# Kernel tuning notes

Measured on AMD Instinct MI355X. Metric: run time of the kernel, lower is better.

The kernel has to match this reference:

```python
import jax, jax.numpy as jnp
import numpy as np

L, V, D, H, F, S = 6, 32000, 768, 12, 3072, 1024
B, T = 2, 1024
DK = D // H
EPS = 1e-5  # torch LayerNorm default


def _ln(x, w, b):
    m = x.mean(-1, keepdims=True)
    v = ((x - m) ** 2).mean(-1, keepdims=True)
    return (x - m) / jnp.sqrt(v + EPS) * w + b


def setup_inputs() -> dict:
    key = jax.random.key(0)
    ks = jax.random.split(key, 16)
    n = lambda k, shape: jax.random.normal(k, shape, jnp.float32) * 0.02
    return {
        "x": jax.random.randint(ks[0], (B, T), 0, V),
        "tok_emb": n(ks[1], (V, D)),
        "pos_emb": n(ks[2], (S, D)),
        "ln1_w": jnp.ones((L, D), jnp.float32), "ln1_b": jnp.zeros((L, D), jnp.float32),
        "wq": n(ks[3], (L, D, D)), "bq": jnp.zeros((L, D), jnp.float32),
        "wk": n(ks[4], (L, D, D)), "bk": jnp.zeros((L, D), jnp.float32),
        "wv": n(ks[5], (L, D, D)), "bv": jnp.zeros((L, D), jnp.float32),
        "wo": n(ks[6], (L, D, D)), "bo": jnp.zeros((L, D), jnp.float32),
        "ln2_w": jnp.ones((L, D), jnp.float32), "ln2_b": jnp.zeros((L, D), jnp.float32),
        "w1": n(ks[7], (L, F, D)), "b1": jnp.zeros((L, F), jnp.float32),
        "w2": n(ks[8], (L, D, F)), "b2": jnp.zeros((L, D), jnp.float32),
        "lnf_w": jnp.ones((D,), jnp.float32), "lnf_b": jnp.zeros((D,), jnp.float32),
        "head_w": n(ks[9], (V, D)),
    }


def reference(x, tok_emb, pos_emb, ln1_w, ln1_b, wq, bq, wk, bk, wv, bv, wo, bo,
              ln2_w, ln2_b, w1, b1, w2, b2, lnf_w, lnf_b, head_w):
    Bx, Tx = x.shape
    h = tok_emb[x] + pos_emb[:Tx]                     # [B,T,D]
    causal = jnp.triu(jnp.ones((Tx, Tx), bool), 1)    # True above diagonal
    scale = 1.0 / np.sqrt(DK)
    for i in range(L):
        a = _ln(h, ln1_w[i], ln1_b[i])
        q = (a @ wq[i].T + bq[i]).reshape(Bx, Tx, H, DK).transpose(0, 2, 1, 3)
        k = (a @ wk[i].T + bk[i]).reshape(Bx, Tx, H, DK).transpose(0, 2, 1, 3)
        v = (a @ wv[i].T + bv[i]).reshape(Bx, Tx, H, DK).transpose(0, 2, 1, 3)
        scores = jnp.einsum("bhtd,bhsd->bhts", q, k) * scale  # [B,H,T,T]
        scores = jnp.where(causal, -jnp.inf, scores)
        attn = jax.nn.softmax(scores, axis=-1)
        ctx = jnp.einsum("bhts,bhsd->bhtd", attn, v)
        ctx = ctx.transpose(0, 2, 1, 3).reshape(Bx, Tx, D)
        h = h + ctx @ wo[i].T + bo[i]
        f = _ln(h, ln2_w[i], ln2_b[i])
        h = h + jax.nn.relu(f @ w1[i].T + b1[i]) @ w2[i].T + b2[i]
    h = _ln(h, lnf_w, lnf_b)
    return h @ head_w.T                               # [B,T,V] logits
```

## Files before the change

kernel.cpp:

```cpp
#include <hip/hip_runtime.h>

typedef unsigned short u16;
typedef __bf16 bf16x8 __attribute__((ext_vector_type(8)));
typedef float f32x4 __attribute__((ext_vector_type(4)));
typedef float f32x4v __attribute__((ext_vector_type(4)));
typedef u16 u16x4 __attribute__((ext_vector_type(4)));

__device__ __forceinline__ float bf2f(u16 u) {
    unsigned x = ((unsigned)u) << 16;
    return __builtin_bit_cast(float, x);
}
__device__ __forceinline__ u16 f2bf(float f) {
    unsigned x = __builtin_bit_cast(unsigned, f);
    unsigned r = (x + 0x7FFFu + ((x >> 16) & 1u)) >> 16;
    return (u16)r;
}

__global__ __launch_bounds__(256) void cvt_kernel(const float* __restrict__ in,
                                                  u16* __restrict__ out, long n,
                                                  long chunk, long stride) {
    for (long i = (long)blockIdx.x * 1024 + (long)threadIdx.x * 4; i < n;
         i += (long)gridDim.x * 1024) {
        f32x4v v = *(const f32x4v*)(in + i);
        u16x4 o;
        o.x = f2bf(v.x); o.y = f2bf(v.y); o.z = f2bf(v.z); o.w = f2bf(v.w);
        long c = i / chunk, rrem = i - c * chunk;
        *(u16x4*)(out + c * stride + rrem) = o;
    }
}

__global__ __launch_bounds__(256) void bias_fuse_kernel(const float* __restrict__ bq,
                                                        const float* __restrict__ bk,
                                                        const float* __restrict__ bv,
                                                        float* __restrict__ dst) {
    int i = blockIdx.x * 256 + threadIdx.x;
    if (i < 6 * 768) {
        int l = i / 768, j = i % 768;
        dst[l * 2304 + j] = bq[i];
        dst[l * 2304 + 768 + j] = bk[i];
        dst[l * 2304 + 1536 + j] = bv[i];
    }
}

__global__ __launch_bounds__(256) void embed_ln_kernel(
    const int* __restrict__ x, const float* __restrict__ tok,
    const float* __restrict__ pos, float* __restrict__ h,
    const float* __restrict__ w, const float* __restrict__ b,
    u16* __restrict__ out) {
    __shared__ float red[4];
    int row = blockIdx.x;
    int t = row & 1023;
    long id = x[row];
    const float* te = tok + id * 768L;
    const float* pe = pos + (long)t * 768L;
    float* hr = h + (long)row * 768L;
    int tid = threadIdx.x, lane = tid & 63, wid = tid >> 6;
    float v0 = te[tid] + pe[tid];
    float v1 = te[tid + 256] + pe[tid + 256];
    float v2 = te[tid + 512] + pe[tid + 512];
    hr[tid] = v0; hr[tid + 256] = v1; hr[tid + 512] = v2;
    float s = v0 + v1 + v2;
    for (int o = 32; o; o >>= 1) s += __shfl_xor(s, o);
    if (lane == 0) red[wid] = s;
    __syncthreads();
    float mean = (red[0] + red[1] + red[2] + red[3]) * (1.f / 768.f);
    __syncthreads();
    float d0 = v0 - mean, d1 = v1 - mean, d2 = v2 - mean;
    float q = d0 * d0 + d1 * d1 + d2 * d2;
    for (int o = 32; o; o >>= 1) q += __shfl_xor(q, o);
    if (lane == 0) red[wid] = q;
    __syncthreads();
    float var = (red[0] + red[1] + red[2] + red[3]) * (1.f / 768.f);
    float rstd = rsqrtf(var + 1e-5f);
    u16* orow = out + (long)row * 768L;
    orow[tid]       = f2bf(d0 * rstd * w[tid]       + b[tid]);
    orow[tid + 256] = f2bf(d1 * rstd * w[tid + 256] + b[tid + 256]);
    orow[tid + 512] = f2bf(d2 * rstd * w[tid + 512] + b[tid + 512]);
}

__global__ __launch_bounds__(192) void redln_kernel(
    const float* __restrict__ part, long pstride, int S,
    const float* __restrict__ bias, float* __restrict__ h,
    const float* __restrict__ w, const float* __restrict__ b,
    u16* __restrict__ out) {
    __shared__ float red[3];
    int row = blockIdx.x;
    int tid = threadIdx.x, lane = tid & 63, wid = tid >> 6;
    long base = (long)row * 768 + tid * 4;
    f32x4v x = *(const f32x4v*)(h + base);
    f32x4v bb = *(const f32x4v*)(bias + tid * 4);
    x += bb;
    for (int s = 0; s < S; s++) x += *(const f32x4v*)(part + (long)s * pstride + base);
    *(f32x4v*)(h + base) = x;
    float s = x.x + x.y + x.z + x.w;
    for (int o = 32; o; o >>= 1) s += __shfl_xor(s, o);
    if (lane == 0) red[wid] = s;
    __syncthreads();
    float mean = (red[0] + red[1] + red[2]) * (1.f / 768.f);
    __syncthreads();
    f32x4v d = x - mean;
    float q = d.x * d.x + d.y * d.y + d.z * d.z + d.w * d.w;
    for (int o = 32; o; o >>= 1) q += __shfl_xor(q, o);
    if (lane == 0) red[wid] = q;
    __syncthreads();
    float var = (red[0] + red[1] + red[2]) * (1.f / 768.f);
    float rstd = rsqrtf(var + 1e-5f);
    f32x4v wv = *(const f32x4v*)(w + tid * 4);
    f32x4v bv = *(const f32x4v*)(b + tid * 4);
    u16x4 o;
    o.x = f2bf(d.x * rstd * wv.x + bv.x);
    o.y = f2bf(d.y * rstd * wv.y + bv.y);
    o.z = f2bf(d.z * rstd * wv.z + bv.z);
    o.w = f2bf(d.w * rstd * wv.w + bv.w);
    *(u16x4*)(out + base) = o;
}

__global__ __launch_bounds__(256) void flash_kernel(
    const u16* __restrict__ qkv,
    const u16* __restrict__ vT,
    u16* __restrict__ ctx) {
    int z = blockIdx.z;
    int zb = z / 12, zh = z - zb * 12;
    int qt = (int)gridDim.x - 1 - (int)blockIdx.x;
    int q0 = qt * 64;
    int tid = threadIdx.x, lane = tid & 63, wid = tid >> 6;
    int rA = lane & 15, sA = lane >> 4;

    const u16* Qbase = qkv + (long)zb * 1024 * 2304 + zh * 64;
    const u16* Kbase = Qbase + 768;
    const u16* Vbase = vT + (long)z * 64 * 1024;

    __shared__ u16 Ks[64 * 64];
    __shared__ u16 Vs[64 * 64];
    __shared__ u16 Ps[4][16 * 64];

    bf16x8 aq[2];
    {
        const u16* qrow = Qbase + (long)(q0 + wid * 16 + rA) * 2304;
        aq[0] = *(const bf16x8*)(qrow + sA * 8);
        aq[1] = *(const bf16x8*)(qrow + 32 + sA * 8);
    }

    float m[4], l[4];
    f32x4 acc_o[4];
#pragma unroll
    for (int j = 0; j < 4; j++) { m[j] = -1e30f; l[j] = 0.f; }
#pragma unroll
    for (int nf = 0; nf < 4; nf++) acc_o[nf] = 0.f;

    int grow0 = q0 + wid * 16 + sA * 4;
    int nkv = qt + 1;
    for (int t = 0; t < nkv; ++t) {
        int kv0 = t * 64;
#pragma unroll
        for (int c0 = 0; c0 < 512; c0 += 256) {
            int c = c0 + tid;
            int row = c >> 3, half = (c >> 2) & 1, sl = c & 3;
            int ks = sl ^ ((row >> 1) & 3);
            __builtin_amdgcn_global_load_lds(
                (const __attribute__((address_space(1))) unsigned*)(Kbase + (long)(kv0 + row) * 2304 + half * 32 + ks * 8),
                (__attribute__((address_space(3))) unsigned*)(Ks + c * 8), 16, 0, 0);
        }
#pragma unroll
        for (int c0 = 0; c0 < 512; c0 += 256) {
            int c = c0 + tid;
            int row = c >> 3, half = (c >> 2) & 1, sl = c & 3;
            int ks = sl ^ ((row >> 1) & 3);
            __builtin_amdgcn_global_load_lds(
                (const __attribute__((address_space(1))) unsigned*)(Vbase + (long)row * 1024 + kv0 + half * 32 + ks * 8),
                (__attribute__((address_space(3))) unsigned*)(Vs + c * 8), 16, 0, 0);
        }
        __syncthreads();

        f32x4 s[4];
#pragma unroll
        for (int nf = 0; nf < 4; nf++) s[nf] = 0.f;
        __builtin_amdgcn_s_setprio(1);
#pragma unroll
        for (int h = 0; h < 2; h++)
#pragma unroll
            for (int nf = 0; nf < 4; nf++) {
                int row = nf * 16 + rA;
                bf16x8 bk_ = *(const bf16x8*)(Ks + row * 64 + h * 32 + ((sA ^ ((row >> 1) & 3))) * 8);
                s[nf] = __builtin_amdgcn_mfma_f32_16x16x32_bf16(aq[h], bk_, s[nf], 0, 0, 0);
            }
        __builtin_amdgcn_s_setprio(0);
#pragma unroll
        for (int nf = 0; nf < 4; nf++) {
            int col = kv0 + nf * 16 + rA;
#pragma unroll
            for (int j = 0; j < 4; j++)
                s[nf][j] = (col <= grow0 + j) ? s[nf][j] * 0.125f : -1e30f;
        }
        float pm[4];
#pragma unroll
        for (int j = 0; j < 4; j++) {
            float v = fmaxf(fmaxf(s[0][j], s[1][j]), fmaxf(s[2][j], s[3][j]));
#pragma unroll
            for (int o = 1; o < 16; o <<= 1) v = fmaxf(v, __shfl_xor(v, o));
            pm[j] = v;
        }
        float esc[4];
#pragma unroll
        for (int j = 0; j < 4; j++) {
            float mn = fmaxf(m[j], pm[j]);
            esc[j] = __expf(m[j] - mn);
            m[j] = mn;
        }
        float ts[4] = {0.f, 0.f, 0.f, 0.f};
#pragma unroll
        for (int nf = 0; nf < 4; nf++) {
            int c = nf * 16 + rA;
            int half = c >> 5, ch = (c >> 3) & 3, e = c & 7;
#pragma unroll
            for (int j = 0; j < 4; j++) {
                float p = __expf(s[nf][j] - m[j]);
                ts[j] += p;
                int r = sA * 4 + j;
                Ps[wid][r * 64 + half * 32 + (ch ^ ((r >> 1) & 3)) * 8 + e] = f2bf(p);
            }
        }
#pragma unroll
        for (int j = 0; j < 4; j++) {
            float v = ts[j];
#pragma unroll
            for (int o = 1; o < 16; o <<= 1) v += __shfl_xor(v, o);
            l[j] = l[j] * esc[j] + v;
        }
#pragma unroll
        for (int nf = 0; nf < 4; nf++)
#pragma unroll
            for (int j = 0; j < 4; j++) acc_o[nf][j] *= esc[j];

        __builtin_amdgcn_s_setprio(1);
#pragma unroll
        for (int h = 0; h < 2; h++) {
            bf16x8 ap = *(const bf16x8*)(Ps[wid] + rA * 64 + h * 32 + ((sA ^ ((rA >> 1) & 3))) * 8);
#pragma unroll
            for (int nf = 0; nf < 4; nf++) {
                int row = nf * 16 + rA;
                bf16x8 bv_ = *(const bf16x8*)(Vs + row * 64 + h * 32 + ((sA ^ ((row >> 1) & 3))) * 8);
                acc_o[nf] = __builtin_amdgcn_mfma_f32_16x16x32_bf16(ap, bv_, acc_o[nf], 0, 0, 0);
            }
        }
        __builtin_amdgcn_s_setprio(0);
        __syncthreads();
    }

    float inv[4];
#pragma unroll
    for (int j = 0; j < 4; j++) inv[j] = 1.f / l[j];
    u16* crow = ctx + ((long)zb * 1024 + q0 + wid * 16) * 768 + zh * 64;
#pragma unroll
    for (int nf = 0; nf < 4; nf++)
#pragma unroll
        for (int j = 0; j < 4; j++)
            crow[(long)(sA * 4 + j) * 768 + nf * 16 + rA] = f2bf(acc_o[nf][j] * inv[j]);
}

template <int BM, int BN, int BK, int EPI, int SK>
__global__ __launch_bounds__(256) void gemm8_kernel(
    const u16* __restrict__ A, int lda,
    const u16* __restrict__ Bm, int ldb,
    void* __restrict__ Cv, int ldc,
    const float* __restrict__ bias, int Kslice, int gm,
    u16* __restrict__ aux, long partStride) {
    constexpr int CPR = BK / 8;
    constexpr int KH = BK / 32;
    int flat = blockIdx.x;
    int tid = threadIdx.x;
    int nwg = gridDim.x;
    int qq = nwg >> 3, rr = nwg & 7;
    int xcd = flat & 7, wi = flat >> 3;
    int swz = (xcd < rr) ? (xcd * (qq + 1) + wi) : (rr * (qq + 1) + (xcd - rr) * qq + wi);
    int slice = 0, wblk = swz;
    if (SK > 1) { int nbs = nwg / SK; slice = swz / nbs; wblk = swz - slice * nbs; }
    int ntile = wblk / gm, mt = wblk - ntile * gm;
    int bm0 = mt * BM, bn0 = ntile * BN;
    long koff = (long)slice * Kslice;
    const u16* Ab = A + (long)bm0 * lda + koff;
    const u16* Bb = Bm + (long)bn0 * ldb + koff;

    __shared__ u16 As[2][BM * BK];
    __shared__ u16 Bs[2][BN * BK];

    int lane = tid & 63, wid = tid >> 6;
    constexpr int WM = BM / 2, WN = BN / 2, MR = WM / 16, NR = WN / 16;
    int wm0 = (wid >> 1) * WM, wn0 = (wid & 1) * WN;

    f32x4 acc[MR][NR];
#pragma unroll
    for (int mi = 0; mi < MR; mi++)
#pragma unroll
        for (int ni = 0; ni < NR; ni++) acc[mi][ni] = 0.f;

    int nt = Kslice / BK;

    auto key = [](int row) { return (BK == 32) ? ((row >> 1) & 3) : (row & 7); };

    auto stage = [&](int buf, int k0) {
        constexpr int CA = BM * CPR;
#pragma unroll
        for (int c0 = 0; c0 < CA; c0 += 256) {
            int c = c0 + tid;
            int row = c / CPR, sl = c & (CPR - 1);
            int ks = sl ^ key(row);
            __builtin_amdgcn_global_load_lds(
                (const __attribute__((address_space(1))) unsigned*)(Ab + (long)row * lda + k0 + ks * 8),
                (__attribute__((address_space(3))) unsigned*)(As[buf] + c * 8), 16, 0, 0);
        }
        constexpr int CB = BN * CPR;
#pragma unroll
        for (int c0 = 0; c0 < CB; c0 += 256) {
            int c = c0 + tid;
            int row = c / CPR, sl = c & (CPR - 1);
            int ks = sl ^ key(row);
            __builtin_amdgcn_global_load_lds(
                (const __attribute__((address_space(1))) unsigned*)(Bb + (long)row * ldb + k0 + ks * 8),
                (__attribute__((address_space(3))) unsigned*)(Bs[buf] + c * 8), 16, 0, 0);
        }
    };

    stage(0, 0);
    __syncthreads();
    int cur = 0;
    int rA = lane & 15, sA = lane >> 4;
    for (int t = 0; t < nt; ++t) {
        if (t + 1 < nt) stage(cur ^ 1, (t + 1) * BK);
        bf16x8 af[MR][KH], bfr[NR][KH];
#pragma unroll
        for (int mi = 0; mi < MR; mi++) {
            int row = wm0 + mi * 16 + rA;
#pragma unroll
            for (int h = 0; h < KH; h++)
                af[mi][h] = *(const bf16x8*)(As[cur] + row * BK + (((h << 2) + sA) ^ key(row)) * 8);
        }
#pragma unroll
        for (int ni = 0; ni < NR; ni++) {
            int row = wn0 + ni * 16 + rA;
#pragma unroll
            for (int h = 0; h < KH; h++)
                bfr[ni][h] = *(const bf16x8*)(Bs[cur] + row * BK + (((h << 2) + sA) ^ key(row)) * 8);
        }
#pragma unroll
        for (int h = 0; h < KH; h++)
#pragma unroll
            for (int mi = 0; mi < MR; mi++)
#pragma unroll
                for (int ni = 0; ni < NR; ni++)
                    acc[mi][ni] = __builtin_amdgcn_mfma_f32_16x16x32_bf16(
                        af[mi][h], bfr[ni][h], acc[mi][ni], 0, 0, 0);
        __syncthreads();
        cur ^= 1;
    }

#pragma unroll
    for (int mi = 0; mi < MR; mi++)
#pragma unroll
        for (int ni = 0; ni < NR; ni++) {
            int gmb = bm0 + wm0 + mi * 16 + ((lane >> 4) << 2);
            int gn = bn0 + wn0 + ni * 16 + (lane & 15);
            if (EPI == 6) {
                if (gn < 1536) {
#pragma unroll
                    for (int j = 0; j < 4; j++)
                        ((u16*)Cv)[(long)(gmb + j) * ldc + gn] =
                            f2bf(acc[mi][ni][j] + bias[gn]);
                } else {
                    u16x4 o;
#pragma unroll
                    for (int j = 0; j < 4; j++) o[j] = f2bf(acc[mi][ni][j] + bias[gn]);
                    int hh = (gn - 1536) >> 6, dk = gn & 63;
                    long off = ((long)((gmb >> 10) * 12 + hh) * 64 + dk) * 1024 + (gmb & 1023);
                    *(u16x4*)(aux + off) = o;
                }
            } else {
#pragma unroll
                for (int j = 0; j < 4; j++) {
                    float v = acc[mi][ni][j];
                    long idx = (long)(gmb + j) * ldc + gn;
                    if (EPI == 2) ((u16*)Cv)[idx] = f2bf(fmaxf(v + bias[gn], 0.f));
                    else ((float*)Cv)[(long)slice * partStride + idx] = v;
                }
            }
        }
}

extern "C" void kernel_launch(void* const* d_in, const int* in_sizes, int n_in,
                              void* d_out, int out_size, void* d_ws, size_t ws_size,
                              hipStream_t stream) {
    const int L = 6, D = 768, F = 3072, T = 1024, V = 32000;
    const int M = 2048;
    const int* x = (const int*)d_in[0];
    const float* tok = (const float*)d_in[1];
    const float* pos = (const float*)d_in[2];
    const float* ln1w = (const float*)d_in[3];
    const float* ln1b = (const float*)d_in[4];
    const float* wq = (const float*)d_in[5];
    const float* bq = (const float*)d_in[6];
    const float* wk = (const float*)d_in[7];
    const float* bk = (const float*)d_in[8];
    const float* wv = (const float*)d_in[9];
    const float* bv = (const float*)d_in[10];
    const float* wo = (const float*)d_in[11];
    const float* bo = (const float*)d_in[12];
    const float* ln2w = (const float*)d_in[13];
    const float* ln2b = (const float*)d_in[14];
    const float* w1 = (const float*)d_in[15];
    const float* b1 = (const float*)d_in[16];
    const float* w2 = (const float*)d_in[17];
    const float* b2 = (const float*)d_in[18];
    const float* lnfw = (const float*)d_in[19];
    const float* lnfb = (const float*)d_in[20];
    const float* headw = (const float*)d_in[21];

    char* p = (char*)d_ws;
    auto alloc = [&](size_t bytes) {
        char* r = p;
        p += (bytes + 255) & ~(size_t)255;
        return r;
    };
    const long DD = (long)D * D, FD = (long)F * D;
    const long PS = (long)M * D;
    u16* qkvw_b = (u16*)alloc(L * 3 * DD * 2);
    u16* wo_b = (u16*)alloc(L * DD * 2);
    u16* w1_b = (u16*)alloc(L * FD * 2);
    u16* w2_b = (u16*)alloc(L * FD * 2);
    u16* hw_b = (u16*)alloc((long)V * D * 2);
    float* qkvbias = (float*)alloc(L * 2304 * 4);
    float* h = (float*)alloc((long)M * D * 4);
    u16* a = (u16*)alloc((long)M * D * 2);
    u16* qkvb = (u16*)alloc((long)M * 2304 * 2);
    u16* vT = (u16*)alloc(24L * 64 * T * 2);
    u16* ctxb = (u16*)alloc((long)M * D * 2);
    u16* f1 = (u16*)alloc((long)M * F * 2);
    float* part = (float*)alloc(4L * PS * 4);

    auto cvt = [&](const float* src, u16* dst, long n, long chunk, long stride) {
        long blocks = (n + 1023) / 1024;
        if (blocks > 4096) blocks = 4096;
        cvt_kernel<<<dim3((unsigned)blocks), 256, 0, stream>>>(src, dst, n, chunk, stride);
    };
    cvt(wq, qkvw_b, L * DD, DD, 3 * DD);
    cvt(wk, qkvw_b + DD, L * DD, DD, 3 * DD);
    cvt(wv, qkvw_b + 2 * DD, L * DD, DD, 3 * DD);
    cvt(wo, wo_b, L * DD, L * DD, L * DD);
    cvt(w1, w1_b, L * FD, L * FD, L * FD);
    cvt(w2, w2_b, L * FD, L * FD, L * FD);
    cvt(headw, hw_b, (long)V * D, (long)V * D, (long)V * D);
    bias_fuse_kernel<<<dim3(18), 256, 0, stream>>>(bq, bk, bv, qkvbias);
    embed_ln_kernel<<<dim3(M), 256, 0, stream>>>(x, tok, pos, h, ln1w, ln1b, a);

    for (int i = 0; i < L; i++) {
        int nx = i + 1;
        bool hn = nx < L;
        gemm8_kernel<64, 128, 64, 6, 1><<<dim3(576), 256, 0, stream>>>(
            a, D, qkvw_b + i * 3 * DD, D, qkvb, 2304, qkvbias + i * 2304,
            D, 32, vT, 0);
        flash_kernel<<<dim3(16, 1, 24), 256, 0, stream>>>(qkvb, vT, ctxb);
        gemm8_kernel<64, 128, 64, 5, 2><<<dim3(384), 256, 0, stream>>>(
            ctxb, D, wo_b + i * DD, D, part, D, nullptr, 384, 32, nullptr, PS);
        redln_kernel<<<dim3(M), 192, 0, stream>>>(
            part, PS, 2, bo + i * D, h, ln2w + i * D, ln2b + i * D, a);
        gemm8_kernel<64, 128, 64, 2, 1><<<dim3(768), 256, 0, stream>>>(
            a, D, w1_b + i * FD, D, f1, F, b1 + i * F, D, 32, nullptr, 0);
        gemm8_kernel<64, 128, 64, 5, 4><<<dim3(768), 256, 0, stream>>>(
            f1, F, w2_b + i * FD, F, part, D, nullptr, 768, 32, nullptr, PS);
        redln_kernel<<<dim3(M), 192, 0, stream>>>(
            part, PS, 4, b2 + i * D, h,
            hn ? ln1w + nx * D : lnfw, hn ? ln1b + nx * D : lnfb, a);
    }
    gemm8_kernel<128, 128, 32, 5, 1><<<dim3(4000), 256, 0, stream>>>(
        a, D, hw_b, D, d_out, V, nullptr, D, 16, nullptr, 0);
}
```

Before: 979.3 us.

## Fuse split-K reduce and LayerNorm into GEMM tail; double-buffer flash K/V

Removes the separate redln kernel and instead has the last-arriving split-K GEMM block for each 64-row tile (tracked by an atomic counter) add the partials, bias and residual, then compute LayerNorm and write bf16 output. It also double-buffers the K/V LDS tiles in the flash attention kernel so the next tile's loads are issued before the current tile is computed. This saves kernel launches and a full pass over h and the partials, and lets global loads overlap with MFMA work. The costs are a serialized tail in one block per row tile, variance computed as E[x²]−mean², and a possible race in the flash kernel because there is no barrier between loading the next tile and reading the current one.

```diff
diff --git a/kernel.cpp b/kernel.cpp
--- a/kernel.cpp
+++ b/kernel.cpp
@@ -78,43 +78,6 @@
     orow[tid + 512] = f2bf(d2 * rstd * w[tid + 512] + b[tid + 512]);
 }
 
-__global__ __launch_bounds__(192) void redln_kernel(
-    const float* __restrict__ part, long pstride, int S,
-    const float* __restrict__ bias, float* __restrict__ h,
-    const float* __restrict__ w, const float* __restrict__ b,
-    u16* __restrict__ out) {
-    __shared__ float red[3];
-    int row = blockIdx.x;
-    int tid = threadIdx.x, lane = tid & 63, wid = tid >> 6;
-    long base = (long)row * 768 + tid * 4;
-    f32x4v x = *(const f32x4v*)(h + base);
-    f32x4v bb = *(const f32x4v*)(bias + tid * 4);
-    x += bb;
-    for (int s = 0; s < S; s++) x += *(const f32x4v*)(part + (long)s * pstride + base);
-    *(f32x4v*)(h + base) = x;
-    float s = x.x + x.y + x.z + x.w;
-    for (int o = 32; o; o >>= 1) s += __shfl_xor(s, o);
-    if (lane == 0) red[wid] = s;
-    __syncthreads();
-    float mean = (red[0] + red[1] + red[2]) * (1.f / 768.f);
-    __syncthreads();
-    f32x4v d = x - mean;
-    float q = d.x * d.x + d.y * d.y + d.z * d.z + d.w * d.w;
-    for (int o = 32; o; o >>= 1) q += __shfl_xor(q, o);
-    if (lane == 0) red[wid] = q;
-    __syncthreads();
-    float var = (red[0] + red[1] + red[2]) * (1.f / 768.f);
-    float rstd = rsqrtf(var + 1e-5f);
-    f32x4v wv = *(const f32x4v*)(w + tid * 4);
-    f32x4v bv = *(const f32x4v*)(b + tid * 4);
-    u16x4 o;
-    o.x = f2bf(d.x * rstd * wv.x + bv.x);
-    o.y = f2bf(d.y * rstd * wv.y + bv.y);
-    o.z = f2bf(d.z * rstd * wv.z + bv.z);
-    o.w = f2bf(d.w * rstd * wv.w + bv.w);
-    *(u16x4*)(out + base) = o;
-}
-
 __global__ __launch_bounds__(256) void flash_kernel(
     const u16* __restrict__ qkv,
     const u16* __restrict__ vT,
@@ -130,8 +93,8 @@
     const u16* Kbase = Qbase + 768;
     const u16* Vbase = vT + (long)z * 64 * 1024;
 
-    __shared__ u16 Ks[64 * 64];
-    __shared__ u16 Vs[64 * 64];
+    __shared__ u16 Ks[2][64 * 64];
+    __shared__ u16 Vs[2][64 * 64];
     __shared__ u16 Ps[4][16 * 64];
 
     bf16x8 aq[2];
@@ -141,17 +104,7 @@
         aq[1] = *(const bf16x8*)(qrow + 32 + sA * 8);
     }
 
-    float m[4], l[4];
-    f32x4 acc_o[4];
-#pragma unroll
-    for (int j = 0; j < 4; j++) { m[j] = -1e30f; l[j] = 0.f; }
-#pragma unroll
-    for (int nf = 0; nf < 4; nf++) acc_o[nf] = 0.f;
-
-    int grow0 = q0 + wid * 16 + sA * 4;
-    int nkv = qt + 1;
-    for (int t = 0; t < nkv; ++t) {
-        int kv0 = t * 64;
+    auto stage = [&](int buf, int kv0) {
 #pragma unroll
         for (int c0 = 0; c0 < 512; c0 += 256) {
             int c = c0 + tid;
@@ -159,7 +112,7 @@
             int ks = sl ^ ((row >> 1) & 3);
             __builtin_amdgcn_global_load_lds(
                 (const __attribute__((address_space(1))) unsigned*)(Kbase + (long)(kv0 + row) * 2304 + half * 32 + ks * 8),
-                (__attribute__((address_space(3))) unsigned*)(Ks + c * 8), 16, 0, 0);
+                (__attribute__((address_space(3))) unsigned*)(Ks[buf] + c * 8), 16, 0, 0);
         }
 #pragma unroll
         for (int c0 = 0; c0 < 512; c0 += 256) {
@@ -168,9 +121,26 @@
             int ks = sl ^ ((row >> 1) & 3);
             __builtin_amdgcn_global_load_lds(
                 (const __attribute__((address_space(1))) unsigned*)(Vbase + (long)row * 1024 + kv0 + half * 32 + ks * 8),
-                (__attribute__((address_space(3))) unsigned*)(Vs + c * 8), 16, 0, 0);
-        }
-        __syncthreads();
+                (__attribute__((address_space(3))) unsigned*)(Vs[buf] + c * 8), 16, 0, 0);
+        }
+    };
+
+    float m[4], l[4];
+    f32x4 acc_o[4];
+#pragma unroll
+    for (int j = 0; j < 4; j++) { m[j] = -1e30f; l[j] = 0.f; }
+#pragma unroll
+    for (int nf = 0; nf < 4; nf++) acc_o[nf] = 0.f;
+
+    int grow0 = q0 + wid * 16 + sA * 4;
+    int nkv = qt + 1;
+
+    stage(0, 0);
+    __syncthreads();
+    for (int t = 0; t < nkv; ++t) {
+        int cur = t & 1;
+        int kv0 = t * 64;
+        if (t + 1 < nkv) stage(cur ^ 1, (t + 1) * 64);
 
         f32x4 s[4];
 #pragma unroll
@@ -181,7 +151,7 @@
 #pragma unroll
             for (int nf = 0; nf < 4; nf++) {
                 int row = nf * 16 + rA;
-                bf16x8 bk_ = *(const bf16x8*)(Ks + row * 64 + h * 32 + ((sA ^ ((row >> 1) & 3))) * 8);
+                bf16x8 bk_ = *(const bf16x8*)(Ks[cur] + row * 64 + h * 32 + ((sA ^ ((row >> 1) & 3))) * 8);
                 s[nf] = __builtin_amdgcn_mfma_f32_16x16x32_bf16(aq[h], bk_, s[nf], 0, 0, 0);
             }
         __builtin_amdgcn_s_setprio(0);
@@ -239,7 +209,7 @@
 #pragma unroll
             for (int nf = 0; nf < 4; nf++) {
                 int row = nf * 16 + rA;
-                bf16x8 bv_ = *(const bf16x8*)(Vs + row * 64 + h * 32 + ((sA ^ ((row >> 1) & 3))) * 8);
+                bf16x8 bv_ = *(const bf16x8*)(Vs[cur] + row * 64 + h * 32 + ((sA ^ ((row >> 1) & 3))) * 8);
                 acc_o[nf] = __builtin_amdgcn_mfma_f32_16x16x32_bf16(ap, bv_, acc_o[nf], 0, 0, 0);
             }
         }
@@ -259,12 +229,16 @@
 }
 
 template <int BM, int BN, int BK, int EPI, int SK>
-__global__ __launch_bounds__(256) void gemm8_kernel(
+__global__ __launch_bounds__(256) void gemm9_kernel(
     const u16* __restrict__ A, int lda,
     const u16* __restrict__ Bm, int ldb,
     void* __restrict__ Cv, int ldc,
     const float* __restrict__ bias, int Kslice, int gm,
-    u16* __restrict__ aux, long partStride) {
+    u16* __restrict__ aux, long partStride,
+    int* __restrict__ cnt, int tailNeed, int tailS,
+    const float* __restrict__ tbias, float* __restrict__ th,
+    const float* __restrict__ tw, const float* __restrict__ tb,
+    u16* __restrict__ tout) {
     constexpr int CPR = BK / 8;
     constexpr int KH = BK / 32;
     int flat = blockIdx.x;
@@ -283,6 +257,7 @@
 
     __shared__ u16 As[2][BM * BK];
     __shared__ u16 Bs[2][BN * BK];
+    __shared__ int isLast;
 
     int lane = tid & 63, wid = tid >> 6;
     constexpr int WM = BM / 2, WN = BN / 2, MR = WM / 16, NR = WN / 16;
@@ -384,6 +359,53 @@
                 }
             }
         }
+
+    if (EPI == 5 && tailNeed > 0) {
+        __syncthreads();
+        if (tid == 0) {
+            __threadfence();
+            int old = atomicAdd(cnt + mt, 1);
+            isLast = (old == tailNeed - 1) ? 1 : 0;
+        }
+        __syncthreads();
+        if (isLast) {
+            __threadfence();
+            const float* part = (const float*)Cv;
+            int r = tid >> 2, sub = tid & 3;
+            long rowbase = (long)(mt * 64 + r) * 768;
+            int col0 = sub * 192;
+            float sum = 0.f, sq = 0.f;
+#pragma unroll 4
+            for (int j = 0; j < 48; j++) {
+                long e = rowbase + col0 + j * 4;
+                f32x4v xv = *(const f32x4v*)(th + e);
+                xv += *(const f32x4v*)(tbias + col0 + j * 4);
+                for (int s = 0; s < tailS; s++)
+                    xv += *(const f32x4v*)(part + (long)s * partStride + e);
+                *(f32x4v*)(th + e) = xv;
+                sum += xv.x + xv.y + xv.z + xv.w;
+                sq += xv.x * xv.x + xv.y * xv.y + xv.z * xv.z + xv.w * xv.w;
+            }
+            sum += __shfl_xor(sum, 1); sum += __shfl_xor(sum, 2);
+            sq += __shfl_xor(sq, 1);  sq += __shfl_xor(sq, 2);
+            float mean = sum * (1.f / 768.f);
+            float var = sq * (1.f / 768.f) - mean * mean;
+            float rstd = rsqrtf(var + 1e-5f);
+#pragma unroll 4
+            for (int j = 0; j < 48; j++) {
+                long e = rowbase + col0 + j * 4;
+                f32x4v xv = *(const f32x4v*)(th + e);
+                f32x4v wv = *(const f32x4v*)(tw + col0 + j * 4);
+                f32x4v bv = *(const f32x4v*)(tb + col0 + j * 4);
+                u16x4 o;
+                o.x = f2bf((xv.x - mean) * rstd * wv.x + bv.x);
+                o.y = f2bf((xv.y - mean) * rstd * wv.y + bv.y);
+                o.z = f2bf((xv.z - mean) * rstd * wv.z + bv.z);
+                o.w = f2bf((xv.w - mean) * rstd * wv.w + bv.w);
+                *(u16x4*)(tout + e) = o;
+            }
+        }
+    }
 }
 
 extern "C" void kernel_launch(void* const* d_in, const int* in_sizes, int n_in,
@@ -435,6 +457,9 @@
     u16* ctxb = (u16*)alloc((long)M * D * 2);
     u16* f1 = (u16*)alloc((long)M * F * 2);
     float* part = (float*)alloc(4L * PS * 4);
+    int* cnts = (int*)alloc(12 * 32 * 4);
+
+    hipMemsetAsync(cnts, 0, 12 * 32 * 4, stream);
 
     auto cvt = [&](const float* src, u16* dst, long n, long chunk, long stride) {
         long blocks = (n + 1023) / 1024;
@@ -454,22 +479,23 @@
     for (int i = 0; i < L; i++) {
         int nx = i + 1;
         bool hn = nx < L;
-        gemm8_kernel<64, 128, 64, 6, 1><<<dim3(576), 256, 0, stream>>>(
+        gemm9_kernel<64, 128, 64, 6, 1><<<dim3(576), 256, 0, stream>>>(
             a, D, qkvw_b + i * 3 * DD, D, qkvb, 2304, qkvbias + i * 2304,
-            D, 32, vT, 0);
+            D, 32, vT, 0, nullptr, 0, 0, nullptr, nullptr, nullptr, nullptr, nullptr);
         flash_kernel<<<dim3(16, 1, 24), 256, 0, stream>>>(qkvb, vT, ctxb);
-        gemm8_kernel<64, 128, 64, 5, 2><<<dim3(384), 256, 0, stream>>>(
-            ctxb, D, wo_b + i * DD, D, part, D, nullptr, 384, 32, nullptr, PS);
-        redln_kernel<<<dim3(M), 192, 0, stream>>>(
-            part, PS, 2, bo + i * D, h, ln2w + i * D, ln2b + i * D, a);
-        gemm8_kernel<64, 128, 64, 2, 1><<<dim3(768), 256, 0, stream>>>(
-            a, D, w1_b + i * FD, D, f1, F, b1 + i * F, D, 32, nullptr, 0);
-        gemm8_kernel<64, 128, 64, 5, 4><<<dim3(768), 256, 0, stream>>>(
-            f1, F, w2_b + i * FD, F, part, D, nullptr, 768, 32, nullptr, PS);
-        redln_kernel<<<dim3(M), 192, 0, stream>>>(
-            part, PS, 4, b2 + i * D, h,
+        gemm9_kernel<64, 128, 64, 5, 2><<<dim3(384), 256, 0, stream>>>(
+            ctxb, D, wo_b + i * DD, D, part, D, nullptr, 384, 32, nullptr, PS,
+            cnts + (i * 2) * 32, 12, 2, bo + i * D, h,
+            ln2w + i * D, ln2b + i * D, a);
+        gemm9_kernel<64, 128, 64, 2, 1><<<dim3(768), 256, 0, stream>>>(
+            a, D, w1_b + i * FD, D, f1, F, b1 + i * F, D, 32, nullptr, 0,
+            nullptr, 0, 0, nullptr, nullptr, nullptr, nullptr, nullptr);
+        gemm9_kernel<64, 128, 64, 5, 4><<<dim3(768), 256, 0, stream>>>(
+            f1, F, w2_b + i * FD, F, part, D, nullptr, 768, 32, nullptr, PS,
+            cnts + (i * 2 + 1) * 32, 24, 4, b2 + i * D, h,
             hn ? ln1w + nx * D : lnfw, hn ? ln1b + nx * D : lnfb, a);
     }
-    gemm8_kernel<128, 128, 32, 5, 1><<<dim3(4000), 256, 0, stream>>>(
-        a, D, hw_b, D, d_out, V, nullptr, D, 16, nullptr, 0);
-}
+    gemm9_kernel<128, 128, 32, 5, 1><<<dim3(4000), 256, 0, stream>>>(
+        a, D, hw_b, D, d_out, V, nullptr, D, 16, nullptr, 0,
+        nullptr, 0, 0, nullptr, nullptr, nullptr, nullptr, nullptr);
+}
```

Measured after the change: 2.137 ms. 118% more time.

## Fuse all transformer layers into one persistent cooperative kernel with grid syncs

Applied to the files above, without the earlier changes.

Replaces the per-layer sequence of QKV GEMM, flash attention, output GEMM, residual-LayerNorm, FFN GEMMs and LayerNorm launches with a single cooperative persistent kernel. Blocks loop over job indices for each stage and call grid.sync between stages. The aim is to remove launch gaps and tail effects across the 42 small launches. The flash attention loop also gains double-buffered K/V staging so the next tile loads while the current one is computed. In exchange it adds grid-wide barrier cost, caps occupancy at a fixed blocks-per-CU value, and forces every stage to share one register and LDS budget.

```diff
diff --git a/kernel.cpp b/kernel.cpp
--- a/kernel.cpp
+++ b/kernel.cpp
@@ -1,4 +1,6 @@
 #include <hip/hip_runtime.h>
+#include <hip/hip_cooperative_groups.h>
+namespace cg = cooperative_groups;
 
 typedef unsigned short u16;
 typedef __bf16 bf16x8 __attribute__((ext_vector_type(8)));
@@ -78,188 +80,11 @@
     orow[tid + 512] = f2bf(d2 * rstd * w[tid + 512] + b[tid + 512]);
 }
 
-__global__ __launch_bounds__(192) void redln_kernel(
-    const float* __restrict__ part, long pstride, int S,
-    const float* __restrict__ bias, float* __restrict__ h,
-    const float* __restrict__ w, const float* __restrict__ b,
-    u16* __restrict__ out) {
-    __shared__ float red[3];
-    int row = blockIdx.x;
-    int tid = threadIdx.x, lane = tid & 63, wid = tid >> 6;
-    long base = (long)row * 768 + tid * 4;
-    f32x4v x = *(const f32x4v*)(h + base);
-    f32x4v bb = *(const f32x4v*)(bias + tid * 4);
-    x += bb;
-    for (int s = 0; s < S; s++) x += *(const f32x4v*)(part + (long)s * pstride + base);
-    *(f32x4v*)(h + base) = x;
-    float s = x.x + x.y + x.z + x.w;
-    for (int o = 32; o; o >>= 1) s += __shfl_xor(s, o);
-    if (lane == 0) red[wid] = s;
-    __syncthreads();
-    float mean = (red[0] + red[1] + red[2]) * (1.f / 768.f);
-    __syncthreads();
-    f32x4v d = x - mean;
-    float q = d.x * d.x + d.y * d.y + d.z * d.z + d.w * d.w;
-    for (int o = 32; o; o >>= 1) q += __shfl_xor(q, o);
-    if (lane == 0) red[wid] = q;
-    __syncthreads();
-    float var = (red[0] + red[1] + red[2]) * (1.f / 768.f);
-    float rstd = rsqrtf(var + 1e-5f);
-    f32x4v wv = *(const f32x4v*)(w + tid * 4);
-    f32x4v bv = *(const f32x4v*)(b + tid * 4);
-    u16x4 o;
-    o.x = f2bf(d.x * rstd * wv.x + bv.x);
-    o.y = f2bf(d.y * rstd * wv.y + bv.y);
-    o.z = f2bf(d.z * rstd * wv.z + bv.z);
-    o.w = f2bf(d.w * rstd * wv.w + bv.w);
-    *(u16x4*)(out + base) = o;
-}
-
-__global__ __launch_bounds__(256) void flash_kernel(
-    const u16* __restrict__ qkv,
-    const u16* __restrict__ vT,
-    u16* __restrict__ ctx) {
-    int z = blockIdx.z;
-    int zb = z / 12, zh = z - zb * 12;
-    int qt = (int)gridDim.x - 1 - (int)blockIdx.x;
-    int q0 = qt * 64;
-    int tid = threadIdx.x, lane = tid & 63, wid = tid >> 6;
-    int rA = lane & 15, sA = lane >> 4;
-
-    const u16* Qbase = qkv + (long)zb * 1024 * 2304 + zh * 64;
-    const u16* Kbase = Qbase + 768;
-    const u16* Vbase = vT + (long)z * 64 * 1024;
-
-    __shared__ u16 Ks[64 * 64];
-    __shared__ u16 Vs[64 * 64];
-    __shared__ u16 Ps[4][16 * 64];
-
-    bf16x8 aq[2];
-    {
-        const u16* qrow = Qbase + (long)(q0 + wid * 16 + rA) * 2304;
-        aq[0] = *(const bf16x8*)(qrow + sA * 8);
-        aq[1] = *(const bf16x8*)(qrow + 32 + sA * 8);
-    }
-
-    float m[4], l[4];
-    f32x4 acc_o[4];
-#pragma unroll
-    for (int j = 0; j < 4; j++) { m[j] = -1e30f; l[j] = 0.f; }
-#pragma unroll
-    for (int nf = 0; nf < 4; nf++) acc_o[nf] = 0.f;
-
-    int grow0 = q0 + wid * 16 + sA * 4;
-    int nkv = qt + 1;
-    for (int t = 0; t < nkv; ++t) {
-        int kv0 = t * 64;
-#pragma unroll
-        for (int c0 = 0; c0 < 512; c0 += 256) {
-            int c = c0 + tid;
-            int row = c >> 3, half = (c >> 2) & 1, sl = c & 3;
-            int ks = sl ^ ((row >> 1) & 3);
-            __builtin_amdgcn_global_load_lds(
-                (const __attribute__((address_space(1))) unsigned*)(Kbase + (long)(kv0 + row) * 2304 + half * 32 + ks * 8),
-                (__attribute__((address_space(3))) unsigned*)(Ks + c * 8), 16, 0, 0);
-        }
-#pragma unroll
-        for (int c0 = 0; c0 < 512; c0 += 256) {
-            int c = c0 + tid;
-            int row = c >> 3, half = (c >> 2) & 1, sl = c & 3;
-            int ks = sl ^ ((row >> 1) & 3);
-            __builtin_amdgcn_global_load_lds(
-                (const __attribute__((address_space(1))) unsigned*)(Vbase + (long)row * 1024 + kv0 + half * 32 + ks * 8),
-                (__attribute__((address_space(3))) unsigned*)(Vs + c * 8), 16, 0, 0);
-        }
-        __syncthreads();
-
-        f32x4 s[4];
-#pragma unroll
-        for (int nf = 0; nf < 4; nf++) s[nf] = 0.f;
-        __builtin_amdgcn_s_setprio(1);
-#pragma unroll
-        for (int h = 0; h < 2; h++)
-#pragma unroll
-            for (int nf = 0; nf < 4; nf++) {
-                int row = nf * 16 + rA;
-                bf16x8 bk_ = *(const bf16x8*)(Ks + row * 64 + h * 32 + ((sA ^ ((row >> 1) & 3))) * 8);
-                s[nf] = __builtin_amdgcn_mfma_f32_16x16x32_bf16(aq[h], bk_, s[nf], 0, 0, 0);
-            }
-        __builtin_amdgcn_s_setprio(0);
-#pragma unroll
-        for (int nf = 0; nf < 4; nf++) {
-            int col = kv0 + nf * 16 + rA;
-#pragma unroll
-            for (int j = 0; j < 4; j++)
-                s[nf][j] = (col <= grow0 + j) ? s[nf][j] * 0.125f : -1e30f;
-        }
-        float pm[4];
-#pragma unroll
-        for (int j = 0; j < 4; j++) {
-            float v = fmaxf(fmaxf(s[0][j], s[1][j]), fmaxf(s[2][j], s[3][j]));
-#pragma unroll
-            for (int o = 1; o < 16; o <<= 1) v = fmaxf(v, __shfl_xor(v, o));
-            pm[j] = v;
-        }
-        float esc[4];
-#pragma unroll
-        for (int j = 0; j < 4; j++) {
-            float mn = fmaxf(m[j], pm[j]);
-            esc[j] = __expf(m[j] - mn);
-            m[j] = mn;
-        }
-        float ts[4] = {0.f, 0.f, 0.f, 0.f};
-#pragma unroll
-        for (int nf = 0; nf < 4; nf++) {
-            int c = nf * 16 + rA;
-            int half = c >> 5, ch = (c >> 3) & 3, e = c & 7;
-#pragma unroll
-            for (int j = 0; j < 4; j++) {
-                float p = __expf(s[nf][j] - m[j]);
-                ts[j] += p;
-                int r = sA * 4 + j;
-                Ps[wid][r * 64 + half * 32 + (ch ^ ((r >> 1) & 3)) * 8 + e] = f2bf(p);
-            }
-        }
-#pragma unroll
-        for (int j = 0; j < 4; j++) {
-            float v = ts[j];
-#pragma unroll
-            for (int o = 1; o < 16; o <<= 1) v += __shfl_xor(v, o);
-            l[j] = l[j] * esc[j] + v;
-        }
-#pragma unroll
-        for (int nf = 0; nf < 4; nf++)
-#pragma unroll
-            for (int j = 0; j < 4; j++) acc_o[nf][j] *= esc[j];
-
-        __builtin_amdgcn_s_setprio(1);
-#pragma unroll
-        for (int h = 0; h < 2; h++) {
-            bf16x8 ap = *(const bf16x8*)(Ps[wid] + rA * 64 + h * 32 + ((sA ^ ((rA >> 1) & 3))) * 8);
-#pragma unroll
-            for (int nf = 0; nf < 4; nf++) {
-                int row = nf * 16 + rA;
-                bf16x8 bv_ = *(const bf16x8*)(Vs + row * 64 + h * 32 + ((sA ^ ((row >> 1) & 3))) * 8);
-                acc_o[nf] = __builtin_amdgcn_mfma_f32_16x16x32_bf16(ap, bv_, acc_o[nf], 0, 0, 0);
-            }
-        }
-        __builtin_amdgcn_s_setprio(0);
-        __syncthreads();
-    }
-
-    float inv[4];
-#pragma unroll
-    for (int j = 0; j < 4; j++) inv[j] = 1.f / l[j];
-    u16* crow = ctx + ((long)zb * 1024 + q0 + wid * 16) * 768 + zh * 64;
-#pragma unroll
-    for (int nf = 0; nf < 4; nf++)
-#pragma unroll
-        for (int j = 0; j < 4; j++)
-            crow[(long)(sA * 4 + j) * 768 + nf * 16 + rA] = f2bf(acc_o[nf][j] * inv[j]);
-}
 
 template <int BM, int BN, int BK, int EPI, int SK>
-__global__ __launch_bounds__(256) void gemm8_kernel(
+__device__ __forceinline__ void gemm_job(
+    int flat, int nwg, int tid,
+    u16* As0, u16* As1, u16* Bs0, u16* Bs1,
     const u16* __restrict__ A, int lda,
     const u16* __restrict__ Bm, int ldb,
     void* __restrict__ Cv, int ldc,
@@ -267,23 +92,17 @@
     u16* __restrict__ aux, long partStride) {
     constexpr int CPR = BK / 8;
     constexpr int KH = BK / 32;
-    int flat = blockIdx.x;
-    int tid = threadIdx.x;
-    int nwg = gridDim.x;
     int qq = nwg >> 3, rr = nwg & 7;
     int xcd = flat & 7, wi = flat >> 3;
     int swz = (xcd < rr) ? (xcd * (qq + 1) + wi) : (rr * (qq + 1) + (xcd - rr) * qq + wi);
     int slice = 0, wblk = swz;
-    if (SK > 1) { int nbs = nwg / SK; slice = swz / nbs; wblk = swz - slice * nbs; }
+    if (SK > 1) { int nbs = nwg / SK; slice = wblk / nbs; wblk -= slice * nbs; }
     int ntile = wblk / gm, mt = wblk - ntile * gm;
     int bm0 = mt * BM, bn0 = ntile * BN;
     long koff = (long)slice * Kslice;
     const u16* Ab = A + (long)bm0 * lda + koff;
     const u16* Bb = Bm + (long)bn0 * ldb + koff;
 
-    __shared__ u16 As[2][BM * BK];
-    __shared__ u16 Bs[2][BN * BK];
-
     int lane = tid & 63, wid = tid >> 6;
     constexpr int WM = BM / 2, WN = BN / 2, MR = WM / 16, NR = WN / 16;
     int wm0 = (wid >> 1) * WM, wn0 = (wid & 1) * WN;
@@ -295,10 +114,8 @@
         for (int ni = 0; ni < NR; ni++) acc[mi][ni] = 0.f;
 
     int nt = Kslice / BK;
-
     auto key = [](int row) { return (BK == 32) ? ((row >> 1) & 3) : (row & 7); };
-
-    auto stage = [&](int buf, int k0) {
+    auto stage = [&](u16* Asb, u16* Bsb, int k0) {
         constexpr int CA = BM * CPR;
 #pragma unroll
         for (int c0 = 0; c0 < CA; c0 += 256) {
@@ -307,7 +124,7 @@
             int ks = sl ^ key(row);
             __builtin_amdgcn_global_load_lds(
                 (const __attribute__((address_space(1))) unsigned*)(Ab + (long)row * lda + k0 + ks * 8),
-                (__attribute__((address_space(3))) unsigned*)(As[buf] + c * 8), 16, 0, 0);
+                (__attribute__((address_space(3))) unsigned*)(Asb + c * 8), 16, 0, 0);
         }
         constexpr int CB = BN * CPR;
 #pragma unroll
@@ -317,30 +134,31 @@
             int ks = sl ^ key(row);
             __builtin_amdgcn_global_load_lds(
                 (const __attribute__((address_space(1))) unsigned*)(Bb + (long)row * ldb + k0 + ks * 8),
-                (__attribute__((address_space(3))) unsigned*)(Bs[buf] + c * 8), 16, 0, 0);
+                (__attribute__((address_space(3))) unsigned*)(Bsb + c * 8), 16, 0, 0);
         }
     };
 
-    stage(0, 0);
-    __syncthreads();
-    int cur = 0;
+    stage(As0, Bs0, 0);
+    __syncthreads();
     int rA = lane & 15, sA = lane >> 4;
     for (int t = 0; t < nt; ++t) {
-        if (t + 1 < nt) stage(cur ^ 1, (t + 1) * BK);
+        u16* Asc = (t & 1) ? As1 : As0;
+        u16* Bsc = (t & 1) ? Bs1 : Bs0;
+        if (t + 1 < nt) stage((t & 1) ? As0 : As1, (t & 1) ? Bs0 : Bs1, (t + 1) * BK);
         bf16x8 af[MR][KH], bfr[NR][KH];
 #pragma unroll
         for (int mi = 0; mi < MR; mi++) {
             int row = wm0 + mi * 16 + rA;
 #pragma unroll
             for (int h = 0; h < KH; h++)
-                af[mi][h] = *(const bf16x8*)(As[cur] + row * BK + (((h << 2) + sA) ^ key(row)) * 8);
+                af[mi][h] = *(const bf16x8*)(Asc + row * BK + (((h << 2) + sA) ^ key(row)) * 8);
         }
 #pragma unroll
         for (int ni = 0; ni < NR; ni++) {
             int row = wn0 + ni * 16 + rA;
 #pragma unroll
             for (int h = 0; h < KH; h++)
-                bfr[ni][h] = *(const bf16x8*)(Bs[cur] + row * BK + (((h << 2) + sA) ^ key(row)) * 8);
+                bfr[ni][h] = *(const bf16x8*)(Bsc + row * BK + (((h << 2) + sA) ^ key(row)) * 8);
         }
 #pragma unroll
         for (int h = 0; h < KH; h++)
@@ -351,7 +169,6 @@
                     acc[mi][ni] = __builtin_amdgcn_mfma_f32_16x16x32_bf16(
                         af[mi][h], bfr[ni][h], acc[mi][ni], 0, 0, 0);
         __syncthreads();
-        cur ^= 1;
     }
 
 #pragma unroll
@@ -384,6 +201,267 @@
                 }
             }
         }
+}
+
+__device__ __forceinline__ void flash_job(
+    int job, int tid, u16* lds,
+    const u16* __restrict__ qkv, const u16* __restrict__ vT,
+    u16* __restrict__ ctx) {
+    int z = job >> 4;
+    int zb = z / 12, zh = z - zb * 12;
+    int qt = 15 - (job & 15);
+    int q0 = qt * 64;
+    int lane = tid & 63, wid = tid >> 6;
+    int rA = lane & 15, sA = lane >> 4;
+
+    u16* Ks0 = lds;            u16* Ks1 = lds + 4096;
+    u16* Vs0 = lds + 8192;     u16* Vs1 = lds + 12288;
+    u16* Psw = lds + 16384 + wid * 1024;
+
+    const u16* Qbase = qkv + (long)zb * 1024 * 2304 + zh * 64;
+    const u16* Kbase = Qbase + 768;
+    const u16* Vbase = vT + (long)z * 64 * 1024;
+
+    bf16x8 aq[2];
+    {
+        const u16* qrow = Qbase + (long)(q0 + wid * 16 + rA) * 2304;
+        aq[0] = *(const bf16x8*)(qrow + sA * 8);
+        aq[1] = *(const bf16x8*)(qrow + 32 + sA * 8);
+    }
+
+    auto stage = [&](u16* Ksb, u16* Vsb, int kv0) {
+#pragma unroll
+        for (int c0 = 0; c0 < 512; c0 += 256) {
+            int c = c0 + tid;
+            int row = c >> 3, half = (c >> 2) & 1, sl = c & 3;
+            int ks = sl ^ ((row >> 1) & 3);
+            __builtin_amdgcn_global_load_lds(
+                (const __attribute__((address_space(1))) unsigned*)(Kbase + (long)(kv0 + row) * 2304 + half * 32 + ks * 8),
+                (__attribute__((address_space(3))) unsigned*)(Ksb + c * 8), 16, 0, 0);
+        }
+#pragma unroll
+        for (int c0 = 0; c0 < 512; c0 += 256) {
+            int c = c0 + tid;
+            int row = c >> 3, half = (c >> 2) & 1, sl = c & 3;
+            int ks = sl ^ ((row >> 1) & 3);
+            __builtin_amdgcn_global_load_lds(
+                (const __attribute__((address_space(1))) unsigned*)(Vbase + (long)row * 1024 + kv0 + half * 32 + ks * 8),
+                (__attribute__((address_space(3))) unsigned*)(Vsb + c * 8), 16, 0, 0);
+        }
+    };
+
+    float m[4], l[4];
+    f32x4 acc_o[4];
+#pragma unroll
+    for (int j = 0; j < 4; j++) { m[j] = -1e30f; l[j] = 0.f; }
+#pragma unroll
+    for (int nf = 0; nf < 4; nf++) acc_o[nf] = 0.f;
+
+    int grow0 = q0 + wid * 16 + sA * 4;
+    int nkv = qt + 1;
+
+    stage(Ks0, Vs0, 0);
+    __syncthreads();
+    for (int t = 0; t < nkv; ++t) {
+        u16* Ksc = (t & 1) ? Ks1 : Ks0;
+        u16* Vsc = (t & 1) ? Vs1 : Vs0;
+        int kv0 = t * 64;
+        if (t + 1 < nkv) stage((t & 1) ? Ks0 : Ks1, (t & 1) ? Vs0 : Vs1, (t + 1) * 64);
+
+        f32x4 s[4];
+#pragma unroll
+        for (int nf = 0; nf < 4; nf++) s[nf] = 0.f;
+        __builtin_amdgcn_s_setprio(1);
+#pragma unroll
+        for (int h = 0; h < 2; h++)
+#pragma unroll
+            for (int nf = 0; nf < 4; nf++) {
+                int row = nf * 16 + rA;
+                bf16x8 bk_ = *(const bf16x8*)(Ksc + row * 64 + h * 32 + ((sA ^ ((row >> 1) & 3))) * 8);
+                s[nf] = __builtin_amdgcn_mfma_f32_16x16x32_bf16(aq[h], bk_, s[nf], 0, 0, 0);
+            }
+        __builtin_amdgcn_s_setprio(0);
+#pragma unroll
+        for (int nf = 0; nf < 4; nf++) {
+            int col = kv0 + nf * 16 + rA;
+#pragma unroll
+            for (int j = 0; j < 4; j++)
+                s[nf][j] = (col <= grow0 + j) ? s[nf][j] * 0.125f : -1e30f;
+        }
+        float pm[4];
+#pragma unroll
+        for (int j = 0; j < 4; j++) {
+            float v = fmaxf(fmaxf(s[0][j], s[1][j]), fmaxf(s[2][j], s[3][j]));
+#pragma unroll
+            for (int o = 1; o < 16; o <<= 1) v = fmaxf(v, __shfl_xor(v, o));
+            pm[j] = v;
+        }
+        float esc[4];
+#pragma unroll
+        for (int j = 0; j < 4; j++) {
+            float mn = fmaxf(m[j], pm[j]);
+            esc[j] = __expf(m[j] - mn);
+            m[j] = mn;
+        }
+        float ts[4] = {0.f, 0.f, 0.f, 0.f};
+#pragma unroll
+        for (int nf = 0; nf < 4; nf++) {
+            int c = nf * 16 + rA;
+            int half = c >> 5, ch = (c >> 3) & 3, e = c & 7;
+#pragma unroll
+            for (int j = 0; j < 4; j++) {
+                float p = __expf(s[nf][j] - m[j]);
+                ts[j] += p;
+                int r = sA * 4 + j;
+                Psw[r * 64 + half * 32 + (ch ^ ((r >> 1) & 3)) * 8 + e] = f2bf(p);
+            }
+        }
+#pragma unroll
+        for (int j = 0; j < 4; j++) {
+            float v = ts[j];
+#pragma unroll
+            for (int o = 1; o < 16; o <<= 1) v += __shfl_xor(v, o);
+            l[j] = l[j] * esc[j] + v;
+        }
+#pragma unroll
+        for (int nf = 0; nf < 4; nf++)
+#pragma unroll
+            for (int j = 0; j < 4; j++) acc_o[nf][j] *= esc[j];
+
+        __builtin_amdgcn_s_setprio(1);
+#pragma unroll
+        for (int h = 0; h < 2; h++) {
+            bf16x8 ap = *(const bf16x8*)(Psw + rA * 64 + h * 32 + ((sA ^ ((rA >> 1) & 3))) * 8);
+#pragma unroll
+            for (int nf = 0; nf < 4; nf++) {
+                int row = nf * 16 + rA;
+                bf16x8 bv_ = *(const bf16x8*)(Vsc + row * 64 + h * 32 + ((sA ^ ((row >> 1) & 3))) * 8);
+                acc_o[nf] = __builtin_amdgcn_mfma_f32_16x16x32_bf16(ap, bv_, acc_o[nf], 0, 0, 0);
+            }
+        }
+        __builtin_amdgcn_s_setprio(0);
+        __syncthreads();
+    }
+
+    float inv[4];
+#pragma unroll
+    for (int j = 0; j < 4; j++) inv[j] = 1.f / l[j];
+    u16* crow = ctx + ((long)zb * 1024 + q0 + wid * 16) * 768 + zh * 64;
+#pragma unroll
+    for (int nf = 0; nf < 4; nf++)
+#pragma unroll
+        for (int j = 0; j < 4; j++)
+            crow[(long)(sA * 4 + j) * 768 + nf * 16 + rA] = f2bf(acc_o[nf][j] * inv[j]);
+}
+
+__device__ __forceinline__ void redln_row(
+    int row, int tid, float* red,
+    const float* __restrict__ part, long pstride, int S,
+    const float* __restrict__ bias, float* __restrict__ h,
+    const float* __restrict__ w, const float* __restrict__ b,
+    u16* __restrict__ out) {
+    int lane = tid & 63, wid = tid >> 6;
+    long base = (long)row * 768;
+    float v[3];
+#pragma unroll
+    for (int j = 0; j < 3; j++) {
+        int e = tid + 256 * j;
+        float x = h[base + e] + bias[e];
+        for (int s = 0; s < S; s++) x += part[(long)s * pstride + base + e];
+        v[j] = x;
+        h[base + e] = x;
+    }
+    float s = v[0] + v[1] + v[2];
+    for (int o = 32; o; o >>= 1) s += __shfl_xor(s, o);
+    if (lane == 0) red[wid] = s;
+    __syncthreads();
+    float mean = (red[0] + red[1] + red[2] + red[3]) * (1.f / 768.f);
+    __syncthreads();
+    float d0 = v[0] - mean, d1 = v[1] - mean, d2 = v[2] - mean;
+    float q = d0 * d0 + d1 * d1 + d2 * d2;
+    for (int o = 32; o; o >>= 1) q += __shfl_xor(q, o);
+    if (lane == 0) red[wid] = q;
+    __syncthreads();
+    float var = (red[0] + red[1] + red[2] + red[3]) * (1.f / 768.f);
+    float rstd = rsqrtf(var + 1e-5f);
+    u16* orow = out + base;
+    orow[tid]       = f2bf(d0 * rstd * w[tid]       + b[tid]);
+    orow[tid + 256] = f2bf(d1 * rstd * w[tid + 256] + b[tid + 256]);
+    orow[tid + 512] = f2bf(d2 * rstd * w[tid + 512] + b[tid + 512]);
+    __syncthreads();
+}
+
+struct LP {
+    const u16* qkvw; const float* qkvbias;
+    u16* a; u16* qkvb; u16* vT; u16* ctxb; u16* f1;
+    const u16* wo; const u16* w1; const u16* w2;
+    const float* bo; const float* b1; const float* b2;
+    const float* ln2w; const float* ln2b;
+    const float* ln1w; const float* ln1b;
+    const float* lnfw; const float* lnfb;
+    float* h; float* part;
+};
+
+__global__ __launch_bounds__(256, 3) void layers_kernel(LP p) {
+    __shared__ u16 lds[24576];
+    cg::grid_group grid = cg::this_grid();
+    int bid = blockIdx.x, tid = threadIdx.x, ng = gridDim.x;
+    const long DD = 768L * 768, FD = 3072L * 768, PS = 2048L * 768;
+    u16* As0 = lds;
+    u16* As1 = lds + 4096;
+    u16* Bs0 = lds + 8192;
+    u16* Bs1 = lds + 16384;
+
+    for (int i = 0; i < 6; ++i) {
+        for (int job = bid; job < 576; job += ng)
+            gemm_job<64, 128, 64, 6, 1>(job, 576, tid, As0, As1, Bs0, Bs1,
+                p.a, 768, p.qkvw + (long)i * 3 * DD, 768, p.qkvb, 2304,
+                p.qkvbias + i * 2304, 768, 32, p.vT, 0);
+        __threadfence(); grid.sync();
+        for (int job = bid; job < 384; job += ng)
+            flash_job(job, tid, lds, p.qkvb, p.vT, p.ctxb);
+        __threadfence(); grid.sync();
+        for (int job = bid; job < 384; job += ng)
+            gemm_job<64, 128, 64, 5, 2>(job, 384, tid, As0, As1, Bs0, Bs1,
+                p.ctxb, 768, p.wo + (long)i * DD, 768, p.part, 768,
+                nullptr, 384, 32, nullptr, PS);
+        __threadfence(); grid.sync();
+        for (int row = bid; row < 2048; row += ng)
+            redln_row(row, tid, (float*)lds, p.part, PS, 2, p.bo + i * 768,
+                      p.h, p.ln2w + i * 768, p.ln2b + i * 768, p.a);
+        __threadfence(); grid.sync();
+        for (int job = bid; job < 768; job += ng)
+            gemm_job<64, 128, 64, 2, 1>(job, 768, tid, As0, As1, Bs0, Bs1,
+                p.a, 768, p.w1 + (long)i * FD, 768, p.f1, 3072,
+                p.b1 + i * 3072, 768, 32, nullptr, 0);
+        __threadfence(); grid.sync();
+        for (int job = bid; job < 768; job += ng)
+            gemm_job<64, 128, 64, 5, 4>(job, 768, tid, As0, As1, Bs0, Bs1,
+                p.f1, 3072, p.w2 + (long)i * FD, 3072, p.part, 768,
+                nullptr, 768, 32, nullptr, PS);
+        __threadfence(); grid.sync();
+        {
+            const float* w = (i + 1 < 6) ? p.ln1w + (i + 1) * 768 : p.lnfw;
+            const float* b = (i + 1 < 6) ? p.ln1b + (i + 1) * 768 : p.lnfb;
+            for (int row = bid; row < 2048; row += ng)
+                redln_row(row, tid, (float*)lds, p.part, PS, 4, p.b2 + i * 768,
+                          p.h, w, b, p.a);
+        }
+        __threadfence(); grid.sync();
+    }
+}
+
+template <int BM, int BN, int BK, int EPI, int SK>
+__global__ __launch_bounds__(256) void gemmg_kernel(
+    const u16* __restrict__ A, int lda,
+    const u16* __restrict__ Bm, int ldb,
+    void* __restrict__ Cv, int ldc,
+    const float* __restrict__ bias, int Kslice, int gm,
+    u16* __restrict__ aux, long partStride) {
+    __shared__ u16 lds[2 * BM * BK + 2 * BN * BK];
+    gemm_job<BM, BN, BK, EPI, SK>(blockIdx.x, gridDim.x, threadIdx.x,
+        lds, lds + BM * BK, lds + 2 * BM * BK, lds + 2 * BM * BK + BN * BK,
+        A, lda, Bm, ldb, Cv, ldc, bias, Kslice, gm, aux, partStride);
 }
 
 extern "C" void kernel_launch(void* const* d_in, const int* in_sizes, int n_in,
@@ -451,25 +529,22 @@
     bias_fuse_kernel<<<dim3(18), 256, 0, stream>>>(bq, bk, bv, qkvbias);
     embed_ln_kernel<<<dim3(M), 256, 0, stream>>>(x, tok, pos, h, ln1w, ln1b, a);
 
-    for (int i = 0; i < L; i++) {
-        int nx = i + 1;
-        bool hn = nx < L;
-        gemm8_kernel<64, 128, 64, 6, 1><<<dim3(576), 256, 0, stream>>>(
-            a, D, qkvw_b + i * 3 * DD, D, qkvb, 2304, qkvbias + i * 2304,
-            D, 32, vT, 0);
-        flash_kernel<<<dim3(16, 1, 24), 256, 0, stream>>>(qkvb, vT, ctxb);
-        gemm8_kernel<64, 128, 64, 5, 2><<<dim3(384), 256, 0, stream>>>(
-            ctxb, D, wo_b + i * DD, D, part, D, nullptr, 384, 32, nullptr, PS);
-        redln_kernel<<<dim3(M), 192, 0, stream>>>(
-            part, PS, 2, bo + i * D, h, ln2w + i * D, ln2b + i * D, a);
-        gemm8_kernel<64, 128, 64, 2, 1><<<dim3(768), 256, 0, stream>>>(
-            a, D, w1_b + i * FD, D, f1, F, b1 + i * F, D, 32, nullptr, 0);
-        gemm8_kernel<64, 128, 64, 5, 4><<<dim3(768), 256, 0, stream>>>(
-            f1, F, w2_b + i * FD, F, part, D, nullptr, 768, 32, nullptr, PS);
-        redln_kernel<<<dim3(M), 192, 0, stream>>>(
-            part, PS, 4, b2 + i * D, h,
-            hn ? ln1w + nx * D : lnfw, hn ? ln1b + nx * D : lnfb, a);
-    }
-    gemm8_kernel<128, 128, 32, 5, 1><<<dim3(4000), 256, 0, stream>>>(
+    LP lp;
+    lp.qkvw = qkvw_b; lp.qkvbias = qkvbias;
+    lp.a = a; lp.qkvb = qkvb; lp.vT = vT; lp.ctxb = ctxb; lp.f1 = f1;
+    lp.wo = wo_b; lp.w1 = w1_b; lp.w2 = w2_b;
+    lp.bo = bo; lp.b1 = b1; lp.b2 = b2;
+    lp.ln2w = ln2w; lp.ln2b = ln2b; lp.ln1w = ln1w; lp.ln1b = ln1b;
+    lp.lnfw = lnfw; lp.lnfb = lnfb;
+    lp.h = h; lp.part = part;
+    int nb = 0;
+    hipOccupancyMaxActiveBlocksPerMultiprocessor(&nb, layers_kernel, 256, 0);
+    if (nb < 1) nb = 1;
+    int grid = nb * 256;
+    if (grid > 768) grid = 768;
+    void* kargs[] = {(void*)&lp};
+    hipLaunchCooperativeKernel(layers_kernel, dim3(grid), dim3(256), kargs, 0, stream);
+
+    gemmg_kernel<128, 128, 32, 5, 1><<<dim3(4000), 256, 0, stream>>>(
         a, D, hw_b, D, d_out, V, nullptr, D, 16, nullptr, 0);
 }
```

Result: slower. 3.577 ms (+265.2%).
